# Performance work log

Measured on AMD Instinct MI355X. Metric: run time of the kernel, lower is better.

## Reference

```python
import jax, jax.numpy as jnp
import numpy as np

N_STATIONS = 100000
N_TIME = 365
N_NEIGHBORS = 5
SMOOTHING = 0.1


def setup_inputs() -> dict:
    key = jax.random.key(0)
    k = jax.random.split(key, 6)
    N, T, K = N_STATIONS, N_TIME, N_NEIGHBORS
    time_vector = jnp.arange(T, dtype=jnp.float32) / 365.25  # years
    constant_offset = jax.random.normal(k[0], (N,), jnp.float32) * 10.0
    linear_trend = jax.random.normal(k[1], (N,), jnp.float32) * 5.0  # mm/yr (ps00_rates buffer)
    seasonal_amplitudes = jax.random.uniform(k[2], (N, 4), jnp.float32) * 6.0
    seasonal_phases = jax.random.uniform(k[3], (N, 4), jnp.float32) * (2.0 * np.pi)
    neighbor_indices = jax.random.randint(k[4], (N, K), 0, N)
    w = jax.random.uniform(k[5], (N, K), jnp.float32) + 1e-3
    neighbor_weights = w / jnp.sum(w, axis=1, keepdims=True)  # row-normalized, like exp-dist weights
    periods = jnp.array([0.25, 0.5, 1.0, 2.0], dtype=jnp.float32)
    return {
        'time_vector': time_vector,
        'constant_offset': constant_offset,
        'linear_trend': linear_trend,
        'seasonal_amplitudes': seasonal_amplitudes,
        'seasonal_phases': seasonal_phases,
        'neighbor_weights': neighbor_weights,
        'periods': periods,
        'neighbor_indices': neighbor_indices,
    }


def _smooth(p, neighbor_indices, neighbor_weights):
    # p: [N, 4]; vectorized version of per-station loop: gather + weighted mean
    nb = p[neighbor_indices]                                   # [N, K, 4]
    avg = jnp.einsum('nkf,nk->nf', nb, neighbor_weights)       # [N, 4]
    return (1.0 - SMOOTHING) * p + SMOOTHING * avg


def reference(time_vector, constant_offset, linear_trend, seasonal_amplitudes,
              seasonal_phases, neighbor_weights, periods, neighbor_indices):
    amps = _smooth(seasonal_amplitudes, neighbor_indices, neighbor_weights)   # [N, 4]
    phs = _smooth(seasonal_phases, neighbor_indices, neighbor_weights)        # [N, 4]
    t = time_vector[None, :]                                                  # [1, T]
    signals = constant_offset[:, None] + linear_trend[:, None] * t           # [N, T]
    two_pi = jnp.float32(2.0 * np.pi)
    for f in range(4):  # fixed small set of seasonal periods
        freq = 1.0 / periods[f]
        signals = signals + amps[:, f:f + 1] * jnp.sin(two_pi * freq * t + phs[:, f:f + 1])
    return signals
```

## Files before the change

### kernel.cpp

```cpp
#include <hip/hip_runtime.h>
#include <math.h>

typedef float f32x2 __attribute__((ext_vector_type(2)));

#define TWO_PI 6.283185307179586f
#define SMOOTH 0.1f
#define SPW 8
#define WAVES 4
#define BLOCK 256
#define SPB (SPW * WAVES)
#define NPAIR 3
#define TP_ROWS 192
#define TP_BYTES (TP_ROWS * 16 * 4)

__device__ __forceinline__ f32x2 sp2(float x) { f32x2 r; r.x = x; r.y = x; return r; }
__device__ __forceinline__ f32x2 mk2(float a, float b) { f32x2 r; r.x = a; r.y = b; return r; }
__device__ __forceinline__ void store8(float* p, f32x2 v) { __builtin_memcpy(p, &v, 8); }
__device__ __forceinline__ float rlane(float v, int l) {
    return __uint_as_float((unsigned)__builtin_amdgcn_readlane((int)__float_as_uint(v), l));
}

__global__ void coef_table_kernel(
    const float* __restrict__ time_vector,
    const float* __restrict__ constant_offset,
    const float* __restrict__ linear_trend,
    const float* __restrict__ amps,
    const float* __restrict__ phs,
    const float* __restrict__ wgt,
    const float* __restrict__ periods,
    const int*   __restrict__ nbidx,
    float* __restrict__ tableP,
    float* __restrict__ coef,
    int N, int T, int K)
{
    int i = blockIdx.x * blockDim.x + threadIdx.x;

    if (i < T) {
        float tv = time_vector[i];
        const int p = i >> 1, o = i & 1;
        float* row = tableP + p * 16;
        #pragma unroll
        for (int f = 0; f < 4; ++f) {
            float ang = (TWO_PI / periods[f]) * tv;
            row[2 * f + o]     = __sinf(ang);
            row[8 + 2 * f + o] = __cosf(ang);
        }
    }

    if (i < N) {
        float4 a = reinterpret_cast<const float4*>(amps)[i];
        float4 p = reinterpret_cast<const float4*>(phs)[i];

        int   nb[5]; float w[5];
        __builtin_memcpy(nb, nbidx + (size_t)i * K, 5 * sizeof(int));
        __builtin_memcpy(w,  wgt   + (size_t)i * K, 5 * sizeof(float));

        float av0 = 0.f, av1 = 0.f, av2 = 0.f, av3 = 0.f;
        float pv0 = 0.f, pv1 = 0.f, pv2 = 0.f, pv3 = 0.f;
        #pragma unroll
        for (int k = 0; k < 5; ++k) {
            float4 na = reinterpret_cast<const float4*>(amps)[nb[k]];
            float4 np = reinterpret_cast<const float4*>(phs)[nb[k]];
            av0 += w[k] * na.x; av1 += w[k] * na.y; av2 += w[k] * na.z; av3 += w[k] * na.w;
            pv0 += w[k] * np.x; pv1 += w[k] * np.y; pv2 += w[k] * np.z; pv3 += w[k] * np.w;
        }
        float sa0 = (1.0f - SMOOTH) * a.x + SMOOTH * av0;
        float sa1 = (1.0f - SMOOTH) * a.y + SMOOTH * av1;
        float sa2 = (1.0f - SMOOTH) * a.z + SMOOTH * av2;
        float sa3 = (1.0f - SMOOTH) * a.w + SMOOTH * av3;
        float sp0 = (1.0f - SMOOTH) * p.x + SMOOTH * pv0;
        float sp1 = (1.0f - SMOOTH) * p.y + SMOOTH * pv1;
        float sp2 = (1.0f - SMOOTH) * p.z + SMOOTH * pv2;
        float sp3 = (1.0f - SMOOTH) * p.w + SMOOTH * pv3;

        float4 vA, vB, vC;
        vA.x = constant_offset[i]; vA.y = linear_trend[i];
        vA.z = sa0 * __cosf(sp0);  vA.w = sa0 * __sinf(sp0);
        vB.x = sa1 * __cosf(sp1);  vB.y = sa1 * __sinf(sp1);
        vB.z = sa2 * __cosf(sp2);  vB.w = sa2 * __sinf(sp2);
        vC.x = sa3 * __cosf(sp3);  vC.y = sa3 * __sinf(sp3);
        vC.z = 0.f; vC.w = 0.f;
        float4* cp = reinterpret_cast<float4*>(coef + (size_t)i * 12);
        cp[0] = vA; cp[1] = vB; cp[2] = vC;
    }
}

__global__ __launch_bounds__(BLOCK) void writer_kernel(
    const float* __restrict__ time_vector,
    const float* __restrict__ tableP,
    const float* __restrict__ coef,
    float* __restrict__ out,
    int N, int T)
{
    const int tid   = threadIdx.x;
    const int wave  = tid >> 6;
    const int lane  = tid & 63;
    const int wbase = blockIdx.x * SPB + wave * SPW;

    if (wbase >= N) return;
    int send = N - wbase; if (send > SPW) send = SPW;

    int sid = wbase + (lane & (SPW - 1));
    if (sid >= N) sid = N - 1;
    const float4* cp = reinterpret_cast<const float4*>(coef + (size_t)sid * 12);
    float4 k0 = cp[0];
    float4 k1 = cp[1];
    float4 k2 = cp[2];

    const int t0 = 2 * lane;
    f32x2 tv[NPAIR];
    f32x2 bs[NPAIR][4], bc[NPAIR][4];
    bool full[NPAIR], any[NPAIR];

    #pragma unroll
    for (int q = 0; q < NPAIR; ++q) {
        const int t = t0 + 128 * q;
        const bool v0 = (t < T), v1 = (t + 1 < T);
        any[q] = v0; full[q] = v1;
        float ta = v0 ? time_vector[t]     : 0.f;
        float tb = v1 ? time_vector[t + 1] : 0.f;
        tv[q] = mk2(ta, tb);

        const float4* rp = reinterpret_cast<const float4*>(tableP + (size_t)(lane + 64 * q) * 16);
        float4 r0 = rp[0];
        float4 r1 = rp[1];
        float4 r2 = rp[2];
        float4 r3 = rp[3];
        bs[q][0] = mk2(r0.x, r0.y); bs[q][1] = mk2(r0.z, r0.w);
        bs[q][2] = mk2(r1.x, r1.y); bs[q][3] = mk2(r1.z, r1.w);
        bc[q][0] = mk2(r2.x, r2.y); bc[q][1] = mk2(r2.z, r2.w);
        bc[q][2] = mk2(r3.x, r3.y); bc[q][3] = mk2(r3.z, r3.w);
    }

    float* obase = out + (size_t)wbase * T;

    #pragma unroll
    for (int j = 0; j < SPW; ++j) {
        if (j >= send) break;
        float sc  = rlane(k0.x, j), sm  = rlane(k0.y, j);
        float sA0 = rlane(k0.z, j), sB0 = rlane(k0.w, j);
        float sA1 = rlane(k1.x, j), sB1 = rlane(k1.y, j);
        float sA2 = rlane(k1.z, j), sB2 = rlane(k1.w, j);
        float sA3 = rlane(k2.x, j), sB3 = rlane(k2.y, j);
        float* orow = obase + (size_t)j * T;

        #pragma unroll
        for (int q = 0; q < NPAIR; ++q) {
            f32x2 sig = sp2(sc) + sp2(sm) * tv[q];
            sig += sp2(sA0) * bs[q][0] + sp2(sB0) * bc[q][0];
            sig += sp2(sA1) * bs[q][1] + sp2(sB1) * bc[q][1];
            sig += sp2(sA2) * bs[q][2] + sp2(sB2) * bc[q][2];
            sig += sp2(sA3) * bs[q][3] + sp2(sB3) * bc[q][3];
            const int t = t0 + 128 * q;
            if (full[q])      store8(orow + t, sig);
            else if (any[q])  orow[t] = sig.x;
        }
    }
}

extern "C" void kernel_launch(void* const* d_in, const int* in_sizes, int n_in,
                              void* d_out, int out_size, void* d_ws, size_t ws_size,
                              hipStream_t stream)
{
    const float* time_vector     = (const float*)d_in[0];
    const float* constant_offset = (const float*)d_in[1];
    const float* linear_trend    = (const float*)d_in[2];
    const float* amps            = (const float*)d_in[3];
    const float* phs             = (const float*)d_in[4];
    const float* wgt             = (const float*)d_in[5];
    const float* periods         = (const float*)d_in[6];
    const int*   nbidx           = (const int*)d_in[7];

    int T = in_sizes[0];
    int N = in_sizes[1];
    int K = in_sizes[5] / N;
    float* out = (float*)d_out;

    float* tableP = (float*)d_ws;
    float* coef   = (float*)((char*)d_ws + TP_BYTES);

    int threads = 256;
    int workA = (N > T) ? N : T;
    int gridA = (workA + threads - 1) / threads;
    coef_table_kernel<<<gridA, threads, 0, stream>>>(
        time_vector, constant_offset, linear_trend, amps, phs, wgt,
        periods, nbidx, tableP, coef, N, T, K);

    int gridW = (N + SPB - 1) / SPB;
    writer_kernel<<<gridW, BLOCK, 0, stream>>>(
        time_vector, tableP, coef, out, N, T);
}
```

Baseline: 42.08 us.

## Stage output rows in LDS and stream contiguous float4 stores from persistent blocks

The writer kernel becomes persistent with a fixed grid of 512 blocks looping over 32-station slabs. Each slab is computed into shared memory and then copied to global memory as fully coalesced float4 stores. Before this, each lane issued strided 8-byte stores across rows of odd length. The sin/cos time table is now computed per thread inside the writer, which removes the table workspace and simplifies the coefficient kernel. The cost is two block barriers per slab, about 46KB of LDS per block (which limits occupancy), and redundant transcendental work in every block.

```diff
diff --git a/kernel.cpp b/kernel.cpp
--- a/kernel.cpp
+++ b/kernel.cpp
@@ -10,104 +10,81 @@
 #define BLOCK 256
 #define SPB (SPW * WAVES)
 #define NPAIR 3
-#define TP_ROWS 192
-#define TP_BYTES (TP_ROWS * 16 * 4)
+#define GRID 512
 
 __device__ __forceinline__ f32x2 sp2(float x) { f32x2 r; r.x = x; r.y = x; return r; }
-__device__ __forceinline__ f32x2 mk2(float a, float b) { f32x2 r; r.x = a; r.y = b; return r; }
-__device__ __forceinline__ void store8(float* p, f32x2 v) { __builtin_memcpy(p, &v, 8); }
 __device__ __forceinline__ float rlane(float v, int l) {
     return __uint_as_float((unsigned)__builtin_amdgcn_readlane((int)__float_as_uint(v), l));
 }
 
-__global__ void coef_table_kernel(
-    const float* __restrict__ time_vector,
+__global__ void coef_kernel(
     const float* __restrict__ constant_offset,
     const float* __restrict__ linear_trend,
     const float* __restrict__ amps,
     const float* __restrict__ phs,
     const float* __restrict__ wgt,
-    const float* __restrict__ periods,
     const int*   __restrict__ nbidx,
-    float* __restrict__ tableP,
     float* __restrict__ coef,
-    int N, int T, int K)
+    int N, int K)
 {
     int i = blockIdx.x * blockDim.x + threadIdx.x;
+    if (i >= N) return;
 
-    if (i < T) {
-        float tv = time_vector[i];
-        const int p = i >> 1, o = i & 1;
-        float* row = tableP + p * 16;
-        #pragma unroll
-        for (int f = 0; f < 4; ++f) {
-            float ang = (TWO_PI / periods[f]) * tv;
-            row[2 * f + o]     = __sinf(ang);
-            row[8 + 2 * f + o] = __cosf(ang);
-        }
+    float4 a = reinterpret_cast<const float4*>(amps)[i];
+    float4 p = reinterpret_cast<const float4*>(phs)[i];
+
+    int   nb[5]; float w[5];
+    __builtin_memcpy(nb, nbidx + (size_t)i * K, 5 * sizeof(int));
+    __builtin_memcpy(w,  wgt   + (size_t)i * K, 5 * sizeof(float));
+
+    float av0 = 0.f, av1 = 0.f, av2 = 0.f, av3 = 0.f;
+    float pv0 = 0.f, pv1 = 0.f, pv2 = 0.f, pv3 = 0.f;
+    #pragma unroll
+    for (int k = 0; k < 5; ++k) {
+        float4 na = reinterpret_cast<const float4*>(amps)[nb[k]];
+        float4 np = reinterpret_cast<const float4*>(phs)[nb[k]];
+        av0 += w[k] * na.x; av1 += w[k] * na.y; av2 += w[k] * na.z; av3 += w[k] * na.w;
+        pv0 += w[k] * np.x; pv1 += w[k] * np.y; pv2 += w[k] * np.z; pv3 += w[k] * np.w;
     }
+    float sa0 = (1.0f - SMOOTH) * a.x + SMOOTH * av0;
+    float sa1 = (1.0f - SMOOTH) * a.y + SMOOTH * av1;
+    float sa2 = (1.0f - SMOOTH) * a.z + SMOOTH * av2;
+    float sa3 = (1.0f - SMOOTH) * a.w + SMOOTH * av3;
+    float sp0 = (1.0f - SMOOTH) * p.x + SMOOTH * pv0;
+    float sp1 = (1.0f - SMOOTH) * p.y + SMOOTH * pv1;
+    float sp2 = (1.0f - SMOOTH) * p.z + SMOOTH * pv2;
+    float sp3 = (1.0f - SMOOTH) * p.w + SMOOTH * pv3;
 
-    if (i < N) {
-        float4 a = reinterpret_cast<const float4*>(amps)[i];
-        float4 p = reinterpret_cast<const float4*>(phs)[i];
-
-        int   nb[5]; float w[5];
-        __builtin_memcpy(nb, nbidx + (size_t)i * K, 5 * sizeof(int));
-        __builtin_memcpy(w,  wgt   + (size_t)i * K, 5 * sizeof(float));
-
-        float av0 = 0.f, av1 = 0.f, av2 = 0.f, av3 = 0.f;
-        float pv0 = 0.f, pv1 = 0.f, pv2 = 0.f, pv3 = 0.f;
-        #pragma unroll
-        for (int k = 0; k < 5; ++k) {
-            float4 na = reinterpret_cast<const float4*>(amps)[nb[k]];
-            float4 np = reinterpret_cast<const float4*>(phs)[nb[k]];
-            av0 += w[k] * na.x; av1 += w[k] * na.y; av2 += w[k] * na.z; av3 += w[k] * na.w;
-            pv0 += w[k] * np.x; pv1 += w[k] * np.y; pv2 += w[k] * np.z; pv3 += w[k] * np.w;
-        }
-        float sa0 = (1.0f - SMOOTH) * a.x + SMOOTH * av0;
-        float sa1 = (1.0f - SMOOTH) * a.y + SMOOTH * av1;
-        float sa2 = (1.0f - SMOOTH) * a.z + SMOOTH * av2;
-        float sa3 = (1.0f - SMOOTH) * a.w + SMOOTH * av3;
-        float sp0 = (1.0f - SMOOTH) * p.x + SMOOTH * pv0;
-        float sp1 = (1.0f - SMOOTH) * p.y + SMOOTH * pv1;
-        float sp2 = (1.0f - SMOOTH) * p.z + SMOOTH * pv2;
-        float sp3 = (1.0f - SMOOTH) * p.w + SMOOTH * pv3;
-
-        float4 vA, vB, vC;
-        vA.x = constant_offset[i]; vA.y = linear_trend[i];
-        vA.z = sa0 * __cosf(sp0);  vA.w = sa0 * __sinf(sp0);
-        vB.x = sa1 * __cosf(sp1);  vB.y = sa1 * __sinf(sp1);
-        vB.z = sa2 * __cosf(sp2);  vB.w = sa2 * __sinf(sp2);
-        vC.x = sa3 * __cosf(sp3);  vC.y = sa3 * __sinf(sp3);
-        vC.z = 0.f; vC.w = 0.f;
-        float4* cp = reinterpret_cast<float4*>(coef + (size_t)i * 12);
-        cp[0] = vA; cp[1] = vB; cp[2] = vC;
-    }
+    float4 vA, vB, vC;
+    vA.x = constant_offset[i]; vA.y = linear_trend[i];
+    vA.z = sa0 * __cosf(sp0);  vA.w = sa0 * __sinf(sp0);
+    vB.x = sa1 * __cosf(sp1);  vB.y = sa1 * __sinf(sp1);
+    vB.z = sa2 * __cosf(sp2);  vB.w = sa2 * __sinf(sp2);
+    vC.x = sa3 * __cosf(sp3);  vC.y = sa3 * __sinf(sp3);
+    vC.z = 0.f; vC.w = 0.f;
+    float4* cp = reinterpret_cast<float4*>(coef + (size_t)i * 12);
+    cp[0] = vA; cp[1] = vB; cp[2] = vC;
 }
 
-__global__ __launch_bounds__(BLOCK) void writer_kernel(
+__global__ __launch_bounds__(BLOCK) void writer_v11(
     const float* __restrict__ time_vector,
-    const float* __restrict__ tableP,
+    const float* __restrict__ periods,
     const float* __restrict__ coef,
     float* __restrict__ out,
-    int N, int T)
+    int N, int T, int nslab)
 {
-    const int tid   = threadIdx.x;
-    const int wave  = tid >> 6;
-    const int lane  = tid & 63;
-    const int wbase = blockIdx.x * SPB + wave * SPW;
+    extern __shared__ float slab[];
 
-    if (wbase >= N) return;
-    int send = N - wbase; if (send > SPW) send = SPW;
+    const int tid  = threadIdx.x;
+    const int wave = tid >> 6;
+    const int lane = tid & 63;
+    const int t0   = 2 * lane;
 
-    int sid = wbase + (lane & (SPW - 1));
-    if (sid >= N) sid = N - 1;
-    const float4* cp = reinterpret_cast<const float4*>(coef + (size_t)sid * 12);
-    float4 k0 = cp[0];
-    float4 k1 = cp[1];
-    float4 k2 = cp[2];
+    const float w0 = TWO_PI / periods[0];
+    const float w1 = TWO_PI / periods[1];
+    const float w2 = TWO_PI / periods[2];
+    const float w3 = TWO_PI / periods[3];
 
-    const int t0 = 2 * lane;
     f32x2 tv[NPAIR];
     f32x2 bs[NPAIR][4], bc[NPAIR][4];
     bool full[NPAIR], any[NPAIR];
@@ -119,42 +96,73 @@
         any[q] = v0; full[q] = v1;
         float ta = v0 ? time_vector[t]     : 0.f;
         float tb = v1 ? time_vector[t + 1] : 0.f;
-        tv[q] = mk2(ta, tb);
-
-        const float4* rp = reinterpret_cast<const float4*>(tableP + (size_t)(lane + 64 * q) * 16);
-        float4 r0 = rp[0];
-        float4 r1 = rp[1];
-        float4 r2 = rp[2];
-        float4 r3 = rp[3];
-        bs[q][0] = mk2(r0.x, r0.y); bs[q][1] = mk2(r0.z, r0.w);
-        bs[q][2] = mk2(r1.x, r1.y); bs[q][3] = mk2(r1.z, r1.w);
-        bc[q][0] = mk2(r2.x, r2.y); bc[q][1] = mk2(r2.z, r2.w);
-        bc[q][2] = mk2(r3.x, r3.y); bc[q][3] = mk2(r3.z, r3.w);
+        f32x2 tvp; tvp.x = ta; tvp.y = tb;
+        tv[q] = tvp;
+        #pragma unroll
+        for (int f = 0; f < 4; ++f) {
+            const float wf = (f == 0) ? w0 : (f == 1) ? w1 : (f == 2) ? w2 : w3;
+            f32x2 s, c;
+            s.x = __sinf(wf * ta); s.y = __sinf(wf * tb);
+            c.x = __cosf(wf * ta); c.y = __cosf(wf * tb);
+            bs[q][f] = s; bc[q][f] = c;
+        }
     }
 
-    float* obase = out + (size_t)wbase * T;
+    for (int i = blockIdx.x; i < nslab; i += GRID) {
+        const int bbase  = i * SPB;
+        const int wfirst = bbase + wave * SPW;
+        const bool fullslab = (bbase + SPB <= N);
 
-    #pragma unroll
-    for (int j = 0; j < SPW; ++j) {
-        if (j >= send) break;
-        float sc  = rlane(k0.x, j), sm  = rlane(k0.y, j);
-        float sA0 = rlane(k0.z, j), sB0 = rlane(k0.w, j);
-        float sA1 = rlane(k1.x, j), sB1 = rlane(k1.y, j);
-        float sA2 = rlane(k1.z, j), sB2 = rlane(k1.w, j);
-        float sA3 = rlane(k2.x, j), sB3 = rlane(k2.y, j);
-        float* orow = obase + (size_t)j * T;
+        int sid = wfirst + (lane & (SPW - 1));
+        if (sid >= N) sid = N - 1;
+        const float4* cp = reinterpret_cast<const float4*>(coef + (size_t)sid * 12);
+        float4 k0 = cp[0];
+        float4 k1 = cp[1];
+        float4 k2 = cp[2];
 
-        #pragma unroll
-        for (int q = 0; q < NPAIR; ++q) {
-            f32x2 sig = sp2(sc) + sp2(sm) * tv[q];
-            sig += sp2(sA0) * bs[q][0] + sp2(sB0) * bc[q][0];
-            sig += sp2(sA1) * bs[q][1] + sp2(sB1) * bc[q][1];
-            sig += sp2(sA2) * bs[q][2] + sp2(sB2) * bc[q][2];
-            sig += sp2(sA3) * bs[q][3] + sp2(sB3) * bc[q][3];
-            const int t = t0 + 128 * q;
-            if (full[q])      store8(orow + t, sig);
-            else if (any[q])  orow[t] = sig.x;
+        int send = N - wfirst; if (send > SPW) send = SPW;
+
+        auto emit_rows = [&](float* rowbase) {
+            #pragma unroll
+            for (int j = 0; j < SPW; ++j) {
+                if (j >= send) break;
+                float sc  = rlane(k0.x, j), sm  = rlane(k0.y, j);
+                float sA0 = rlane(k0.z, j), sB0 = rlane(k0.w, j);
+                float sA1 = rlane(k1.x, j), sB1 = rlane(k1.y, j);
+                float sA2 = rlane(k1.z, j), sB2 = rlane(k1.w, j);
+                float sA3 = rlane(k2.x, j), sB3 = rlane(k2.y, j);
+                float* row = rowbase + (size_t)j * T;
+                #pragma unroll
+                for (int q = 0; q < NPAIR; ++q) {
+                    f32x2 sig = sp2(sc) + sp2(sm) * tv[q];
+                    sig += sp2(sA0) * bs[q][0] + sp2(sB0) * bc[q][0];
+                    sig += sp2(sA1) * bs[q][1] + sp2(sB1) * bc[q][1];
+                    sig += sp2(sA2) * bs[q][2] + sp2(sB2) * bc[q][2];
+                    sig += sp2(sA3) * bs[q][3] + sp2(sB3) * bc[q][3];
+                    const int t = t0 + 128 * q;
+                    if (full[q]) { row[t] = sig.x; row[t + 1] = sig.y; }
+                    else if (any[q]) { row[t] = sig.x; }
+                }
+            }
+        };
+
+        if (fullslab) {
+            emit_rows(slab + (size_t)(wave * SPW) * T);
+        } else if (send > 0) {
+            emit_rows(out + (size_t)wfirst * T);
         }
+
+        __syncthreads();
+
+        if (fullslab) {
+            const float4* lsrc = reinterpret_cast<const float4*>(slab);
+            float4* gdst = reinterpret_cast<float4*>(out + (size_t)bbase * T);
+            const int nch = (SPB * T) >> 2;
+            for (int c = tid; c < nch; c += BLOCK)
+                gdst[c] = lsrc[c];
+        }
+
+        __syncthreads();
     }
 }
 
@@ -176,17 +184,14 @@
     int K = in_sizes[5] / N;
     float* out = (float*)d_out;
 
-    float* tableP = (float*)d_ws;
-    float* coef   = (float*)((char*)d_ws + TP_BYTES);
+    float* coef = (float*)d_ws;
 
-    int threads = 256;
-    int workA = (N > T) ? N : T;
-    int gridA = (workA + threads - 1) / threads;
-    coef_table_kernel<<<gridA, threads, 0, stream>>>(
-        time_vector, constant_offset, linear_trend, amps, phs, wgt,
-        periods, nbidx, tableP, coef, N, T, K);
+    int gridA = (N + 255) / 256;
+    coef_kernel<<<gridA, 256, 0, stream>>>(
+        constant_offset, linear_trend, amps, phs, wgt, nbidx, coef, N, K);
 
-    int gridW = (N + SPB - 1) / SPB;
-    writer_kernel<<<gridW, BLOCK, 0, stream>>>(
-        time_vector, tableP, coef, out, N, T);
+    int nslab = (N + SPB - 1) / SPB;
+    size_t shmem = (size_t)SPB * T * sizeof(float);
+    writer_v11<<<GRID, BLOCK, shmem, stream>>>(
+        time_vector, periods, coef, out, N, T, nslab);
 }
```

Result: slower. 43.63 us (+3.7%).

## Stage writer output in LDS and emit coalesced nontemporal 16-byte stores

Applied to the files above, without the earlier changes.

The writer kernel now computes each block's 32 rows into a shared-memory slab. After a barrier it copies the slab to global memory as contiguous float4 nontemporal stores. This replaces the scattered 8-byte stores, which were misaligned because the row length is odd. A template specialisation for T=365 unrolls the copy loop. The cost is about 46KB of LDS per block, which lowers occupancy, plus an extra LDS round-trip and a __syncthreads.

```diff
diff --git a/kernel.cpp b/kernel.cpp
--- a/kernel.cpp
+++ b/kernel.cpp
@@ -2,6 +2,7 @@
 #include <math.h>
 
 typedef float f32x2 __attribute__((ext_vector_type(2)));
+typedef float f32x4 __attribute__((ext_vector_type(4)));
 
 #define TWO_PI 6.283185307179586f
 #define SMOOTH 0.1f
@@ -15,7 +16,6 @@
 
 __device__ __forceinline__ f32x2 sp2(float x) { f32x2 r; r.x = x; r.y = x; return r; }
 __device__ __forceinline__ f32x2 mk2(float a, float b) { f32x2 r; r.x = a; r.y = b; return r; }
-__device__ __forceinline__ void store8(float* p, f32x2 v) { __builtin_memcpy(p, &v, 8); }
 __device__ __forceinline__ float rlane(float v, int l) {
     return __uint_as_float((unsigned)__builtin_amdgcn_readlane((int)__float_as_uint(v), l));
 }
@@ -85,20 +85,25 @@
     }
 }
 
-__global__ __launch_bounds__(BLOCK) void writer_kernel(
+template<int TT>
+__global__ __launch_bounds__(BLOCK) void writer_v15(
     const float* __restrict__ time_vector,
     const float* __restrict__ tableP,
     const float* __restrict__ coef,
     float* __restrict__ out,
-    int N, int T)
+    int N, int T_rt)
 {
-    const int tid   = threadIdx.x;
-    const int wave  = tid >> 6;
-    const int lane  = tid & 63;
-    const int wbase = blockIdx.x * SPB + wave * SPW;
-
-    if (wbase >= N) return;
-    int send = N - wbase; if (send > SPW) send = SPW;
+    const int T = (TT > 0) ? TT : T_rt;
+    extern __shared__ float slab[];
+
+    const int tid    = threadIdx.x;
+    const int wave   = tid >> 6;
+    const int lane   = tid & 63;
+    const int bbase  = blockIdx.x * SPB;
+    const int wbase  = bbase + wave * SPW;
+
+    if (bbase >= N) return;
+    int bsend = N - bbase; if (bsend > SPB) bsend = SPB;
 
     int sid = wbase + (lane & (SPW - 1));
     if (sid >= N) sid = N - 1;
@@ -132,28 +137,88 @@
         bc[q][2] = mk2(r3.x, r3.y); bc[q][3] = mk2(r3.z, r3.w);
     }
 
-    float* obase = out + (size_t)wbase * T;
-
-    #pragma unroll
-    for (int j = 0; j < SPW; ++j) {
-        if (j >= send) break;
-        float sc  = rlane(k0.x, j), sm  = rlane(k0.y, j);
-        float sA0 = rlane(k0.z, j), sB0 = rlane(k0.w, j);
-        float sA1 = rlane(k1.x, j), sB1 = rlane(k1.y, j);
-        float sA2 = rlane(k1.z, j), sB2 = rlane(k1.w, j);
-        float sA3 = rlane(k2.x, j), sB3 = rlane(k2.y, j);
-        float* orow = obase + (size_t)j * T;
+    if (bsend == SPB) {
+        float* wrows = slab + (size_t)(wave * SPW) * T;
 
         #pragma unroll
-        for (int q = 0; q < NPAIR; ++q) {
-            f32x2 sig = sp2(sc) + sp2(sm) * tv[q];
-            sig += sp2(sA0) * bs[q][0] + sp2(sB0) * bc[q][0];
-            sig += sp2(sA1) * bs[q][1] + sp2(sB1) * bc[q][1];
-            sig += sp2(sA2) * bs[q][2] + sp2(sB2) * bc[q][2];
-            sig += sp2(sA3) * bs[q][3] + sp2(sB3) * bc[q][3];
-            const int t = t0 + 128 * q;
-            if (full[q])      store8(orow + t, sig);
-            else if (any[q])  orow[t] = sig.x;
+        for (int j = 0; j < SPW; ++j) {
+            float sc  = rlane(k0.x, j), sm  = rlane(k0.y, j);
+            float sA0 = rlane(k0.z, j), sB0 = rlane(k0.w, j);
+            float sA1 = rlane(k1.x, j), sB1 = rlane(k1.y, j);
+            float sA2 = rlane(k1.z, j), sB2 = rlane(k1.w, j);
+            float sA3 = rlane(k2.x, j), sB3 = rlane(k2.y, j);
+            float* lrow = wrows + j * T;
+
+            #pragma unroll
+            for (int q = 0; q < NPAIR; ++q) {
+                f32x2 sig = sp2(sc) + sp2(sm) * tv[q];
+                sig += sp2(sA0) * bs[q][0] + sp2(sB0) * bc[q][0];
+                sig += sp2(sA1) * bs[q][1] + sp2(sB1) * bc[q][1];
+                sig += sp2(sA2) * bs[q][2] + sp2(sB2) * bc[q][2];
+                sig += sp2(sA3) * bs[q][3] + sp2(sB3) * bc[q][3];
+                const int t = t0 + 128 * q;
+                if (full[q]) { lrow[t] = sig.x; lrow[t + 1] = sig.y; }
+                else if (any[q]) { lrow[t] = sig.x; }
+            }
+        }
+
+        __syncthreads();
+
+        const f32x4* lsrc = reinterpret_cast<const f32x4*>(slab);
+        f32x4* gdst = reinterpret_cast<f32x4*>(out + (size_t)bbase * T);
+
+        if (TT == 365) {
+            f32x4 v0_ = lsrc[tid];          f32x4 v1_ = lsrc[tid + 256];
+            f32x4 v2_ = lsrc[tid + 512];    f32x4 v3_ = lsrc[tid + 768];
+            f32x4 v4_ = lsrc[tid + 1024];   f32x4 v5_ = lsrc[tid + 1280];
+            f32x4 v6_ = lsrc[tid + 1536];   f32x4 v7_ = lsrc[tid + 1792];
+            f32x4 v8_ = lsrc[tid + 2048];   f32x4 v9_ = lsrc[tid + 2304];
+            f32x4 va_ = lsrc[tid + 2560];
+            const bool extra = (tid < 104);
+            f32x4 vb_;
+            if (extra) vb_ = lsrc[tid + 2816];
+
+            __builtin_nontemporal_store(v0_, gdst + tid);
+            __builtin_nontemporal_store(v1_, gdst + tid + 256);
+            __builtin_nontemporal_store(v2_, gdst + tid + 512);
+            __builtin_nontemporal_store(v3_, gdst + tid + 768);
+            __builtin_nontemporal_store(v4_, gdst + tid + 1024);
+            __builtin_nontemporal_store(v5_, gdst + tid + 1280);
+            __builtin_nontemporal_store(v6_, gdst + tid + 1536);
+            __builtin_nontemporal_store(v7_, gdst + tid + 1792);
+            __builtin_nontemporal_store(v8_, gdst + tid + 2048);
+            __builtin_nontemporal_store(v9_, gdst + tid + 2304);
+            __builtin_nontemporal_store(va_, gdst + tid + 2560);
+            if (extra) __builtin_nontemporal_store(vb_, gdst + tid + 2816);
+        } else {
+            const int nch = (SPB * T) >> 2;
+            for (int i = tid; i < nch; i += BLOCK) {
+                f32x4 v = lsrc[i];
+                __builtin_nontemporal_store(v, gdst + i);
+            }
+        }
+    } else {
+        int send = N - wbase; if (send > SPW) send = SPW;
+        if (send <= 0) return;
+        float* obase = out + (size_t)wbase * T;
+        for (int j = 0; j < send; ++j) {
+            float sc  = rlane(k0.x, j), sm  = rlane(k0.y, j);
+            float sA0 = rlane(k0.z, j), sB0 = rlane(k0.w, j);
+            float sA1 = rlane(k1.x, j), sB1 = rlane(k1.y, j);
+            float sA2 = rlane(k1.z, j), sB2 = rlane(k1.w, j);
+            float sA3 = rlane(k2.x, j), sB3 = rlane(k2.y, j);
+            float* orow = obase + (size_t)j * T;
+            #pragma unroll
+            for (int q = 0; q < NPAIR; ++q) {
+                f32x2 sig = sp2(sc) + sp2(sm) * tv[q];
+                sig += sp2(sA0) * bs[q][0] + sp2(sB0) * bc[q][0];
+                sig += sp2(sA1) * bs[q][1] + sp2(sB1) * bc[q][1];
+                sig += sp2(sA2) * bs[q][2] + sp2(sB2) * bc[q][2];
+                sig += sp2(sA3) * bs[q][3] + sp2(sB3) * bc[q][3];
+                const int t = t0 + 128 * q;
+                if (full[q]) { orow[t] = sig.x; orow[t + 1] = sig.y; }
+                else if (any[q]) { orow[t] = sig.x; }
+            }
         }
     }
 }
@@ -186,7 +251,13 @@
         time_vector, constant_offset, linear_trend, amps, phs, wgt,
         periods, nbidx, tableP, coef, N, T, K);
 
-    int gridW = (N + SPB - 1) / SPB;
-    writer_kernel<<<gridW, BLOCK, 0, stream>>>(
-        time_vector, tableP, coef, out, N, T);
-}
+    int grid = (N + SPB - 1) / SPB;
+    size_t shmem = (size_t)SPB * T * sizeof(float);
+    if (T == 365) {
+        writer_v15<365><<<grid, BLOCK, shmem, stream>>>(
+            time_vector, tableP, coef, out, N, T);
+    } else {
+        writer_v15<0><<<grid, BLOCK, shmem, stream>>>(
+            time_vector, tableP, coef, out, N, T);
+    }
+}
```

Result: slower. 44.09 us (+4.8%).
